# Optimization experiments

Measured on AMD Instinct MI355X. Metric: run time of the kernel, lower is better.

Reference implementation:

```python
import jax, jax.numpy as jnp
import numpy as np

B, S, D_IN = 2, 2048, 1024
D_OUT, HEADS = 1024, 16
HD = D_OUT // HEADS  # head_dim = 64


def rope_sincos(seq_len, head_dim):
    half = head_dim // 2
    inv_freq = 1.0 / (10000.0 ** (jnp.arange(half, dtype=jnp.float32) / half))
    angles = jnp.arange(seq_len, dtype=jnp.float32)[:, None] * inv_freq[None, :]  # (s, hd/2)
    return jnp.sin(angles), jnp.cos(angles)


def apply_rope(x, sin, cos):
    # x: (b, h, s, hd); interleaved-pair rotation as in the torch module
    b, h, s, hd = x.shape
    xp = x.reshape(b, h, s, hd // 2, 2)
    x0, x1 = xp[..., 0], xp[..., 1]
    sin = sin[:s][None, None, :, :]
    cos = cos[:s][None, None, :, :]
    r0 = x0 * cos - x1 * sin
    r1 = x0 * sin + x1 * cos
    return jnp.stack([r0, r1], axis=-1).reshape(b, h, s, hd)


def setup_inputs() -> dict:
    key = jax.random.key(0)
    kx, kq, kk, kv, ko = jax.random.split(key, 5)
    scale = 0.02
    return {
        "x": jax.random.normal(kx, (B, S, D_IN), dtype=jnp.float32),
        "Wq": jax.random.normal(kq, (D_IN, D_OUT), dtype=jnp.float32) * scale,
        "Wk": jax.random.normal(kk, (D_IN, D_OUT), dtype=jnp.float32) * scale,
        "Wv": jax.random.normal(kv, (D_IN, D_OUT), dtype=jnp.float32) * scale,
        "Wo": jax.random.normal(ko, (D_OUT, D_OUT), dtype=jnp.float32) * scale,
    }


def reference(x, Wq, Wk, Wv, Wo):
    b, s, _ = x.shape
    q = (x @ Wq).reshape(b, s, HEADS, HD).transpose(0, 2, 1, 3)  # (b,h,s,hd)
    k = (x @ Wk).reshape(b, s, HEADS, HD).transpose(0, 2, 1, 3)
    v = (x @ Wv).reshape(b, s, HEADS, HD).transpose(0, 2, 1, 3)
    sin, cos = rope_sincos(s, HD)
    q = apply_rope(q, sin, cos)
    k = apply_rope(k, sin, cos)
    scores = jnp.einsum('bhqd,bhkd->bhqk', q, k)
    causal = jnp.triu(jnp.ones((s, s), dtype=bool), 1)
    scores = jnp.where(causal[None, None], -jnp.inf, scores)
    weights = jax.nn.softmax(scores / jnp.sqrt(jnp.float32(HD)), axis=-1)
    ctx = jnp.einsum('bhqk,bhkd->bhqd', weights, v)
    ctx = ctx.transpose(0, 2, 1, 3).reshape(b, s, D_OUT)
    return ctx @ Wo
```

## Files before the change

kernel.cpp:

```cpp
#include <hip/hip_runtime.h>
#include <cstdint>
#include <cstddef>

#define BB 2
#define SS 2048
#define DD 1024
#define HH 16
#define HDD 64

typedef unsigned short u16;
typedef unsigned int u32;
typedef __attribute__((ext_vector_type(8))) short bf16x8;
typedef __attribute__((ext_vector_type(4))) float f32x4;

__device__ __forceinline__ u16 f2bf(float f) {
    union { float f; u32 u; } c; c.f = f;
    u32 r = c.u + 0x7fffu + ((c.u >> 16) & 1u);
    return (u16)(r >> 16);
}
__device__ __forceinline__ void gll16(const void* g, void* l) {
    __builtin_amdgcn_global_load_lds(
        (const __attribute__((address_space(1))) void*)g,
        (__attribute__((address_space(3))) void*)l, 16, 0, 0);
}

__global__ __launch_bounds__(256) void cvt_x(const float* __restrict__ X, u16* __restrict__ Xb)
{
    const int idx0 = blockIdx.x * 256 + threadIdx.x;
    #pragma unroll
    for (int i = 0; i < 4; i++) {
        const int c = idx0 + i * 262144;
        const float4 v = *(const float4*)&X[(size_t)c * 4];
        ushort4 o;
        o.x = f2bf(v.x); o.y = f2bf(v.y); o.z = f2bf(v.z); o.w = f2bf(v.w);
        *(ushort4*)&Xb[(size_t)c * 4] = o;
    }
}

__global__ __launch_bounds__(256) void trans_w4(
    const float* Wq, const float* Wk, const float* Wv, const float* Wo,
    u16* __restrict__ WTbase)
{
    __shared__ float L[32][33];
    const float* Ws[4] = {Wq, Wk, Wv, Wo};
    const float* W = Ws[blockIdx.z];
    u16* WT = WTbase + (size_t)blockIdx.z * (DD * DD);
    const int k0 = blockIdx.x * 32, n0 = blockIdx.y * 32;
    const int tx = threadIdx.x & 31, ty = threadIdx.x >> 5;
    #pragma unroll
    for (int i = 0; i < 4; i++)
        L[ty + 8 * i][tx] = W[(size_t)(k0 + ty + 8 * i) * DD + n0 + tx];
    __syncthreads();
    #pragma unroll
    for (int i = 0; i < 4; i++) {
        const int n = ty + 8 * i;
        WT[(size_t)(n0 + n) * DD + k0 + tx] = f2bf(L[tx][n]);
    }
}

__global__ __launch_bounds__(256) void gemm_qkv(
    const u16* __restrict__ Xb, const u16* __restrict__ WTall, u16* __restrict__ QKVb)
{
    __shared__ __align__(16) u16 sm[16384];
    const int tid = threadIdx.x;
    const int lane = tid & 63;
    const int w = tid >> 6;
    const int li = lane & 15, quad = lane >> 4;
    const int wr = w >> 1, wc = w & 1;
    const int which = blockIdx.x >> 3;
    const int n0 = (blockIdx.x & 7) * 128;
    const int m0 = blockIdx.y * 64;
    const u16* BT = WTall + (size_t)which * (DD * DD);
    u16* outp = QKVb + (size_t)which * ((size_t)BB * HH * SS * HDD);
    const float scale = (which == 0) ? 0.125f * 1.4426950408889634f : 1.0f;

    const int arow = tid >> 2;
    const int acol = (tid & 3) * 8;
    const int wbase = (tid >> 6) * 1024;

    auto stage = [&](int t, int buf) {
        char* base = (char*)(sm + buf * 6144);
        const int k0 = t * 32;
        gll16(Xb + (size_t)(m0 + arow) * DD + k0 + acol, base + wbase);
        #pragma unroll
        for (int rr = 0; rr < 2; rr++)
            gll16(BT + (size_t)(n0 + rr * 64 + arow) * DD + k0 + acol,
                  base + 4096 + rr * 4096 + wbase);
    };

    f32x4 acc[2][4] = {};
    stage(0, 0);
    __syncthreads();
    for (int t = 0; t < 32; t++) {
        const int buf = t & 1;
        if (t < 31) stage(t + 1, buf ^ 1);
        const u16* tA = sm + buf * 6144;
        const u16* tB = tA + 2048;
        bf16x8 a[2], b[4];
        #pragma unroll
        for (int f = 0; f < 2; f++)
            a[f] = *(const bf16x8*)(tA + (wr * 32 + f * 16 + li) * 32 + quad * 8);
        #pragma unroll
        for (int f = 0; f < 4; f++)
            b[f] = *(const bf16x8*)(tB + (wc * 64 + f * 16 + li) * 32 + quad * 8);
        #pragma unroll
        for (int fm = 0; fm < 2; fm++)
            #pragma unroll
            for (int fn = 0; fn < 4; fn++)
                acc[fm][fn] = __builtin_amdgcn_mfma_f32_16x16x32_bf16(
                    a[fm], b[fn], acc[fm][fn], 0, 0, 0);
        __syncthreads();
    }

    const int bidx = m0 >> 11;
    const int s0 = m0 & (SS - 1);
    if (which < 2) {
        float* tabc = (float*)(sm + 8192);
        float* tabs = tabc + 2048;
        {
            const int j = tid & 31;
            const int sb = tid >> 5;
            const float inv = exp2f((float)j * -0.4152410118609203f);
            #pragma unroll
            for (int k = 0; k < 8; k++) {
                const int sl = k * 8 + sb;
                float sn, cs;
                sincosf((float)(s0 + sl) * inv, &sn, &cs);
                tabc[sl * 32 + j] = cs;
                tabs[sl * 32 + j] = sn;
            }
        }
        float (*Ts)[128] = (float(*)[128])sm;
        #pragma unroll
        for (int p = 0; p < 2; p++) {
            if (p) __syncthreads();
            if (wr == p) {
                #pragma unroll
                for (int fm = 0; fm < 2; fm++)
                    #pragma unroll
                    for (int fn = 0; fn < 4; fn++)
                        #pragma unroll
                        for (int r = 0; r < 4; r++)
                            Ts[fm * 16 + quad * 4 + r][wc * 64 + fn * 16 + li] = acc[fm][fn][r];
            }
            __syncthreads();
            #pragma unroll
            for (int i = 0; i < 2; i++) {
                const int c = tid + 256 * i;
                const int mr = c >> 4;
                const int nc = c & 15;
                const int sl = p * 32 + mr;
                const int s = s0 + sl;
                const int n = n0 + nc * 8;
                const int h = n >> 6, hd0 = n & 63;
                const int j0 = hd0 >> 1;
                const float4 v0 = *(const float4*)&Ts[mr][nc * 8];
                const float4 v1 = *(const float4*)&Ts[mr][nc * 8 + 4];
                const float4 cs4 = *(const float4*)&tabc[sl * 32 + j0];
                const float4 sn4 = *(const float4*)&tabs[sl * 32 + j0];
                u32 w0, w1, w2, w3;
                w0 = (u32)f2bf((v0.x * cs4.x - v0.y * sn4.x) * scale) |
                     ((u32)f2bf((v0.x * sn4.x + v0.y * cs4.x) * scale) << 16);
                w1 = (u32)f2bf((v0.z * cs4.y - v0.w * sn4.y) * scale) |
                     ((u32)f2bf((v0.z * sn4.y + v0.w * cs4.y) * scale) << 16);
                w2 = (u32)f2bf((v1.x * cs4.z - v1.y * sn4.z) * scale) |
                     ((u32)f2bf((v1.x * sn4.z + v1.y * cs4.z) * scale) << 16);
                w3 = (u32)f2bf((v1.z * cs4.w - v1.w * sn4.w) * scale) |
                     ((u32)f2bf((v1.z * sn4.w + v1.w * cs4.w) * scale) << 16);
                uint4 ov; ov.x = w0; ov.y = w1; ov.z = w2; ov.w = w3;
                *(uint4*)&outp[((size_t)(bidx * HH + h) * SS + s) * HDD + hd0] = ov;
            }
        }
    } else {
        float (*Ts)[64] = (float(*)[64])sm;
        #pragma unroll
        for (int fm = 0; fm < 2; fm++)
            #pragma unroll
            for (int fn = 0; fn < 4; fn++)
                *(float4*)&Ts[wc * 64 + fn * 16 + li][wr * 32 + fm * 16 + quad * 4] =
                    make_float4(acc[fm][fn][0], acc[fm][fn][1],
                                acc[fm][fn][2], acc[fm][fn][3]);
        __syncthreads();
        #pragma unroll
        for (int i = 0; i < 4; i++) {
            const int c = tid + 256 * i;
            const int nr = c >> 3;
            const int mc = c & 7;
            const int n = n0 + nr;
            const int h = n >> 6, hd = n & 63;
            const float4 v0 = *(const float4*)&Ts[nr][mc * 8];
            const float4 v1 = *(const float4*)&Ts[nr][mc * 8 + 4];
            uint4 ov;
            ov.x = (u32)f2bf(v0.x) | ((u32)f2bf(v0.y) << 16);
            ov.y = (u32)f2bf(v0.z) | ((u32)f2bf(v0.w) << 16);
            ov.z = (u32)f2bf(v1.x) | ((u32)f2bf(v1.y) << 16);
            ov.w = (u32)f2bf(v1.z) | ((u32)f2bf(v1.w) << 16);
            *(uint4*)&outp[((size_t)(bidx * HH + h) * HDD + hd) * SS + s0 + mc * 8] = ov;
        }
    }
}

__global__ __launch_bounds__(512) void attn_mfma(
    const u16* __restrict__ Qb, const u16* __restrict__ Kb,
    const u16* __restrict__ Vt, u16* __restrict__ ctxb)
{
    __shared__ u16 Ks[128][72];
    __shared__ u16 Vs[64][136];
    __shared__ u16 Ps[8][16][136];
    const int tid = threadIdx.x;
    const int lane = tid & 63;
    const int w = tid >> 6;
    const int li = lane & 15;
    const int quad = lane >> 4;
    const int bh = blockIdx.y;
    const int i = blockIdx.x;
    const int q0A = 128 * i;
    const int q0B = 128 * (15 - i);
    const int ntA = i + 1;
    const int ntB = 16 - i;

    bf16x8 aQA0, aQA1, aQB0, aQB1;
    {
        const u16* qa = Qb + ((size_t)bh * SS + q0A + 16 * w + li) * HDD + quad * 8;
        aQA0 = *(const bf16x8*)qa;
        aQA1 = *(const bf16x8*)(qa + 32);
        const u16* qb = Qb + ((size_t)bh * SS + q0B + 16 * w + li) * HDD + quad * 8;
        aQB0 = *(const bf16x8*)qb;
        aQB1 = *(const bf16x8*)(qb + 32);
    }

    f32x4 OA[4] = {}, OB[4] = {};
    float lA[4] = {}, lB[4] = {};

    const int kr = tid >> 2;
    const int kc = (tid & 3) * 16;
    const int vr = tid >> 3;
    const int vc = (tid & 7) * 16;

    auto process = [&](const bf16x8& aQ0, const bf16x8& aQ1,
                       f32x4 (&O)[4], float (&l_r)[4], const bool diag) {
        f32x4 S[8];
        #pragma unroll
        for (int t = 0; t < 8; t++) {
            const bf16x8 b0 = *(const bf16x8*)&Ks[16 * t + li][quad * 8];
            const bf16x8 b1 = *(const bf16x8*)&Ks[16 * t + li][32 + quad * 8];
            f32x4 a2 = {};
            a2 = __builtin_amdgcn_mfma_f32_16x16x32_bf16(aQ0, b0, a2, 0, 0, 0);
            a2 = __builtin_amdgcn_mfma_f32_16x16x32_bf16(aQ1, b1, a2, 0, 0, 0);
            S[t] = a2;
        }
        if (diag) {
            #pragma unroll
            for (int t = 0; t < 8; t++)
                #pragma unroll
                for (int r = 0; r < 4; r++)
                    if (16 * t + li > 16 * w + quad * 4 + r) S[t][r] = -1e30f;
        }
        float p[4][8];
        #pragma unroll
        for (int r = 0; r < 4; r++) {
            float ls = 0.f;
            #pragma unroll
            for (int t = 0; t < 8; t++) {
                p[r][t] = exp2f(S[t][r] - 8.0f);
                ls += p[r][t];
            }
            l_r[r] += ls;
        }
        #pragma unroll
        for (int r = 0; r < 4; r++)
            #pragma unroll
            for (int t = 0; t < 8; t++)
                Ps[w][quad * 4 + r][16 * t + li] = f2bf(p[r][t]);
        bf16x8 aP[4];
        #pragma unroll
        for (int c = 0; c < 4; c++)
            aP[c] = *(const bf16x8*)&Ps[w][li][32 * c + quad * 8];
        #pragma unroll
        for (int t2 = 0; t2 < 4; t2++) {
            #pragma unroll
            for (int c = 0; c < 4; c++) {
                const bf16x8 bv = *(const bf16x8*)&Vs[16 * t2 + li][32 * c + quad * 8];
                O[t2] = __builtin_amdgcn_mfma_f32_16x16x32_bf16(aP[c], bv, O[t2], 0, 0, 0);
            }
        }
    };

    for (int jt = 0; jt < ntB; jt++) {
        const int j0 = jt << 7;
        const uint4 k0v = *(const uint4*)(Kb + ((size_t)bh * SS + j0 + kr) * HDD + kc);
        const uint4 k1v = *(const uint4*)(Kb + ((size_t)bh * SS + j0 + kr) * HDD + kc + 8);
        const uint4 v0v = *(const uint4*)(Vt + ((size_t)bh * HDD + vr) * SS + j0 + vc);
        const uint4 v1v = *(const uint4*)(Vt + ((size_t)bh * HDD + vr) * SS + j0 + vc + 8);
        __syncthreads();
        *(uint4*)&Ks[kr][kc] = k0v;
        *(uint4*)&Ks[kr][kc + 8] = k1v;
        *(uint4*)&Vs[vr][vc] = v0v;
        *(uint4*)&Vs[vr][vc + 8] = v1v;
        __syncthreads();

        if (jt < ntA) process(aQA0, aQA1, OA, lA, jt == ntA - 1);
        process(aQB0, aQB1, OB, lB, jt == ntB - 1);
    }

    const int b = bh >> 4, h = bh & 15;
    #pragma unroll
    for (int r = 0; r < 4; r++) {
        float la = lA[r], lb = lB[r];
        #pragma unroll
        for (int off = 1; off < 16; off <<= 1) {
            la += __shfl_xor(la, off);
            lb += __shfl_xor(lb, off);
        }
        const float invA = 1.f / la;
        const float invB = 1.f / lb;
        const int rowA = q0A + 16 * w + quad * 4 + r;
        const int rowB = q0B + 16 * w + quad * 4 + r;
        #pragma unroll
        for (int t2 = 0; t2 < 4; t2++) {
            ctxb[((size_t)b * SS + rowA) * DD + h * HDD + 16 * t2 + li] = f2bf(OA[t2][r] * invA);
            ctxb[((size_t)b * SS + rowB) * DD + h * HDD + 16 * t2 + li] = f2bf(OB[t2][r] * invB);
        }
    }
}

__global__ __launch_bounds__(256) void gemm_out_mfma(
    const u16* __restrict__ Ab, const u16* __restrict__ WoT, float* __restrict__ out)
{
    __shared__ __align__(16) u16 sm[12288];
    const int tid = threadIdx.x;
    const int lane = tid & 63;
    const int w = tid >> 6;
    const int li = lane & 15, quad = lane >> 4;
    const int wr = w >> 1, wc = w & 1;
    const int n0 = blockIdx.x * 128;
    const int m0 = blockIdx.y * 64;

    const int arow = tid >> 2;
    const int acol = (tid & 3) * 8;
    const int wbase = (tid >> 6) * 1024;

    auto stage = [&](int t, int buf) {
        char* base = (char*)(sm + buf * 6144);
        const int k0 = t * 32;
        gll16(Ab + (size_t)(m0 + arow) * DD + k0 + acol, base + wbase);
        #pragma unroll
        for (int rr = 0; rr < 2; rr++)
            gll16(WoT + (size_t)(n0 + rr * 64 + arow) * DD + k0 + acol,
                  base + 4096 + rr * 4096 + wbase);
    };

    f32x4 acc[2][4] = {};
    stage(0, 0);
    __syncthreads();
    for (int t = 0; t < 32; t++) {
        const int buf = t & 1;
        if (t < 31) stage(t + 1, buf ^ 1);
        const u16* tA = sm + buf * 6144;
        const u16* tB = tA + 2048;
        bf16x8 a[2], b[4];
        #pragma unroll
        for (int f = 0; f < 2; f++)
            a[f] = *(const bf16x8*)(tA + (wr * 32 + f * 16 + li) * 32 + quad * 8);
        #pragma unroll
        for (int f = 0; f < 4; f++)
            b[f] = *(const bf16x8*)(tB + (wc * 64 + f * 16 + li) * 32 + quad * 8);
        #pragma unroll
        for (int fm = 0; fm < 2; fm++)
            #pragma unroll
            for (int fn = 0; fn < 4; fn++)
                acc[fm][fn] = __builtin_amdgcn_mfma_f32_16x16x32_bf16(
                    a[fm], b[fn], acc[fm][fn], 0, 0, 0);
        __syncthreads();
    }

    #pragma unroll
    for (int fm = 0; fm < 2; fm++)
        #pragma unroll
        for (int r = 0; r < 4; r++) {
            const size_t mg = (size_t)(m0 + wr * 32 + fm * 16 + quad * 4 + r) * DD;
            #pragma unroll
            for (int fn = 0; fn < 4; fn++)
                out[mg + n0 + wc * 64 + fn * 16 + li] = acc[fm][fn][r];
        }
}

extern "C" void kernel_launch(void* const* d_in, const int* in_sizes, int n_in,
                              void* d_out, int out_size, void* d_ws, size_t ws_size,
                              hipStream_t stream) {
    const float* x  = (const float*)d_in[0];
    const float* Wq = (const float*)d_in[1];
    const float* Wk = (const float*)d_in[2];
    const float* Wv = (const float*)d_in[3];
    const float* Wo = (const float*)d_in[4];
    float* out = (float*)d_out;

    u16* ws16 = (u16*)d_ws;
    const size_t E = 4194304;
    const size_t M = 1048576;
    u16* QKVb = ws16;
    u16* Qb   = QKVb;
    u16* Kb   = QKVb + E;
    u16* Vt   = QKVb + 2 * E;
    u16* Xb   = ws16 + 3 * E;
    u16* ctxb = Xb;
    u16* WTall = ws16 + 4 * E;
    u16* WoT  = WTall + 3 * M;

    hipLaunchKernelGGL(cvt_x, dim3(1024), dim3(256), 0, stream, x, Xb);
    hipLaunchKernelGGL(trans_w4, dim3(32, 32, 4), dim3(256), 0, stream,
                       Wq, Wk, Wv, Wo, WTall);
    hipLaunchKernelGGL(gemm_qkv, dim3(24, 64), dim3(256), 0, stream, Xb, WTall, QKVb);
    hipLaunchKernelGGL(attn_mfma, dim3(8, BB * HH), dim3(512), 0, stream,
                       Qb, Kb, Vt, ctxb);
    hipLaunchKernelGGL(gemm_out_mfma, dim3(8, 64), dim3(256), 0, stream, ctxb, WoT, out);
}
```

Measured before the change: 204.7 us.

## Merge prep kernels, reorder attention grid, raise wave priority around MFMA

Combines the X conversion and the weight transposes into one launch, using z index 4 for the X cast, which removes one kernel launch and its gap. Swaps the attention grid axes so consecutive blocks cover different heads, which changes dispatch order and load balance across CUs. Adds s_setprio around the MFMA sections so waves doing matrix math get issue priority over waves doing softmax. The merged kernel keeps a __syncthreads inside a branch that depends only on the block index, so it stays uniform per block.

After: 202.2 us. Within noise of the previous version (-1.2%).

```diff
diff --git a/kernel.cpp b/kernel.cpp
--- a/kernel.cpp
+++ b/kernel.cpp
@@ -24,37 +24,38 @@
         (__attribute__((address_space(3))) void*)l, 16, 0, 0);
 }
 
-__global__ __launch_bounds__(256) void cvt_x(const float* __restrict__ X, u16* __restrict__ Xb)
-{
-    const int idx0 = blockIdx.x * 256 + threadIdx.x;
-    #pragma unroll
-    for (int i = 0; i < 4; i++) {
-        const int c = idx0 + i * 262144;
-        const float4 v = *(const float4*)&X[(size_t)c * 4];
-        ushort4 o;
-        o.x = f2bf(v.x); o.y = f2bf(v.y); o.z = f2bf(v.z); o.w = f2bf(v.w);
-        *(ushort4*)&Xb[(size_t)c * 4] = o;
-    }
-}
-
-__global__ __launch_bounds__(256) void trans_w4(
-    const float* Wq, const float* Wk, const float* Wv, const float* Wo,
-    u16* __restrict__ WTbase)
+__global__ __launch_bounds__(256) void prep_all(
+    const float* X, const float* Wq, const float* Wk, const float* Wv, const float* Wo,
+    u16* Xb, u16* WTbase)
 {
     __shared__ float L[32][33];
-    const float* Ws[4] = {Wq, Wk, Wv, Wo};
-    const float* W = Ws[blockIdx.z];
-    u16* WT = WTbase + (size_t)blockIdx.z * (DD * DD);
-    const int k0 = blockIdx.x * 32, n0 = blockIdx.y * 32;
-    const int tx = threadIdx.x & 31, ty = threadIdx.x >> 5;
-    #pragma unroll
-    for (int i = 0; i < 4; i++)
-        L[ty + 8 * i][tx] = W[(size_t)(k0 + ty + 8 * i) * DD + n0 + tx];
-    __syncthreads();
-    #pragma unroll
-    for (int i = 0; i < 4; i++) {
-        const int n = ty + 8 * i;
-        WT[(size_t)(n0 + n) * DD + k0 + tx] = f2bf(L[tx][n]);
+    const int z = blockIdx.z;
+    if (z < 4) {
+        const float* Ws[4] = {Wq, Wk, Wv, Wo};
+        const float* W = Ws[z];
+        u16* WT = WTbase + (size_t)z * (DD * DD);
+        const int k0 = blockIdx.x * 32, n0 = blockIdx.y * 32;
+        const int tx = threadIdx.x & 31, ty = threadIdx.x >> 5;
+        #pragma unroll
+        for (int i = 0; i < 4; i++)
+            L[ty + 8 * i][tx] = W[(size_t)(k0 + ty + 8 * i) * DD + n0 + tx];
+        __syncthreads();
+        #pragma unroll
+        for (int i = 0; i < 4; i++) {
+            const int n = ty + 8 * i;
+            WT[(size_t)(n0 + n) * DD + k0 + tx] = f2bf(L[tx][n]);
+        }
+    } else {
+        const int bid = blockIdx.x + 32 * blockIdx.y;
+        const int idx0 = bid * 256 + threadIdx.x;
+        #pragma unroll
+        for (int i = 0; i < 4; i++) {
+            const int c = idx0 + i * 262144;
+            const float4 v = *(const float4*)&X[(size_t)c * 4];
+            ushort4 o;
+            o.x = f2bf(v.x); o.y = f2bf(v.y); o.z = f2bf(v.z); o.w = f2bf(v.w);
+            *(ushort4*)&Xb[(size_t)c * 4] = o;
+        }
     }
 }
 
@@ -212,8 +213,8 @@
     const int w = tid >> 6;
     const int li = lane & 15;
     const int quad = lane >> 4;
-    const int bh = blockIdx.y;
-    const int i = blockIdx.x;
+    const int bh = blockIdx.x;
+    const int i = blockIdx.y;
     const int q0A = 128 * i;
     const int q0B = 128 * (15 - i);
     const int ntA = i + 1;
@@ -240,6 +241,7 @@
     auto process = [&](const bf16x8& aQ0, const bf16x8& aQ1,
                        f32x4 (&O)[4], float (&l_r)[4], const bool diag) {
         f32x4 S[8];
+        __builtin_amdgcn_s_setprio(1);
         #pragma unroll
         for (int t = 0; t < 8; t++) {
             const bf16x8 b0 = *(const bf16x8*)&Ks[16 * t + li][quad * 8];
@@ -249,6 +251,7 @@
             a2 = __builtin_amdgcn_mfma_f32_16x16x32_bf16(aQ1, b1, a2, 0, 0, 0);
             S[t] = a2;
         }
+        __builtin_amdgcn_s_setprio(0);
         if (diag) {
             #pragma unroll
             for (int t = 0; t < 8; t++)
@@ -276,6 +279,7 @@
         #pragma unroll
         for (int c = 0; c < 4; c++)
             aP[c] = *(const bf16x8*)&Ps[w][li][32 * c + quad * 8];
+        __builtin_amdgcn_s_setprio(1);
         #pragma unroll
         for (int t2 = 0; t2 < 4; t2++) {
             #pragma unroll
@@ -284,6 +288,7 @@
                 O[t2] = __builtin_amdgcn_mfma_f32_16x16x32_bf16(aP[c], bv, O[t2], 0, 0, 0);
             }
         }
+        __builtin_amdgcn_s_setprio(0);
     };
 
     for (int jt = 0; jt < ntB; jt++) {
@@ -407,11 +412,10 @@
     u16* WTall = ws16 + 4 * E;
     u16* WoT  = WTall + 3 * M;
 
-    hipLaunchKernelGGL(cvt_x, dim3(1024), dim3(256), 0, stream, x, Xb);
-    hipLaunchKernelGGL(trans_w4, dim3(32, 32, 4), dim3(256), 0, stream,
-                       Wq, Wk, Wv, Wo, WTall);
+    hipLaunchKernelGGL(prep_all, dim3(32, 32, 5), dim3(256), 0, stream,
+                       x, Wq, Wk, Wv, Wo, Xb, WTall);
     hipLaunchKernelGGL(gemm_qkv, dim3(24, 64), dim3(256), 0, stream, Xb, WTall, QKVb);
-    hipLaunchKernelGGL(attn_mfma, dim3(8, BB * HH), dim3(512), 0, stream,
+    hipLaunchKernelGGL(attn_mfma, dim3(BB * HH, 8), dim3(512), 0, stream,
                        Qb, Kb, Vt, ctxb);
     hipLaunchKernelGGL(gemm_out_mfma, dim3(8, 64), dim3(256), 0, stream, ctxb, WoT, out);
 }
```
